# Performance work log

Hardware: AMD Instinct MI355X
Metric: run time of the kernel (lower is better)

## Reference

```python
import jax, jax.numpy as jnp
import numpy as np
from jax import lax
from jax.scipy.special import logsumexp

B, T, H, L = 64, 512, 768, 9


def setup_inputs() -> dict:
    key = jax.random.key(0)
    k1, k2, k3, k4, k5 = jax.random.split(key, 5)
    hidden = jax.random.normal(k1, (B, T, H), dtype=jnp.float32)
    W = jax.random.normal(k2, (L, H), dtype=jnp.float32) * 0.02
    b = jnp.zeros((L,), dtype=jnp.float32)
    transitions = jax.random.normal(k3, (L, L), dtype=jnp.float32) * 0.1
    lengths = jax.random.randint(k4, (B,), T // 2, T + 1)
    seq_mask = jnp.arange(T)[None, :] < lengths[:, None]          # [B,T] bool
    labels = jax.random.randint(k5, (B, T), 0, L).astype(jnp.int32)
    labels = jnp.where(seq_mask, labels, -100).astype(jnp.int32)   # -100 = ignore
    attention_mask = seq_mask.astype(jnp.int32)
    return {"hidden": hidden, "W": W, "b": b, "transitions": transitions,
            "labels": labels, "attention_mask": attention_mask}


def _crf_nll(logits, tags, transitions, mask):
    # numerator: joint score of the gold path (no start/end transitions)
    maskf = mask.astype(logits.dtype)
    emit = jnp.take_along_axis(logits, tags[..., None], axis=2)[..., 0]   # [B,T]
    emit_score = (emit * maskf).sum(-1)
    trans = transitions[tags[:, :-1], tags[:, 1:]]                        # [B,T-1]
    trans_score = (trans * maskf[:, 1:]).sum(-1)
    numerator = emit_score + trans_score
    # denominator: forward algorithm (log-sum-exp recurrence over time)
    def step(alpha, xs):
        logit_t, mask_t = xs                                   # [B,L], [B]
        inner = alpha[:, :, None] + transitions[None, :, :] + logit_t[:, None, :]
        new = logsumexp(inner, axis=1)
        return jnp.where(mask_t[:, None], new, alpha), None
    alpha0 = logits[:, 0]                                      # mask[:,0] assumed True
    alpha, _ = lax.scan(step, alpha0,
                        (jnp.transpose(logits[:, 1:], (1, 0, 2)), mask[:, 1:].T))
    denominator = logsumexp(alpha, axis=-1)
    return -(numerator - denominator).sum()


def _viterbi(logits, transitions, mask):
    num_tags = transitions.shape[0]
    identity_bp = jnp.broadcast_to(jnp.arange(num_tags)[None, :], logits.shape[:1] + (num_tags,))

    def vstep(vscore, xs):
        logit_t, mask_t = xs
        inner = vscore[:, :, None] + transitions[None, :, :]   # [B,L_prev,L_cur]
        bp = jnp.argmax(inner, axis=1)                         # [B,L]
        new = jnp.max(inner, axis=1) + logit_t
        vscore = jnp.where(mask_t[:, None], new, vscore)
        bp = jnp.where(mask_t[:, None], bp, identity_bp)       # carry tag through pad
        return vscore, bp

    vscore0 = logits[:, 0]
    vscore, bps = lax.scan(vstep, vscore0,
                           (jnp.transpose(logits[:, 1:], (1, 0, 2)), mask[:, 1:].T))
    last_tag = jnp.argmax(vscore, axis=-1)                     # [B]

    def btstep(tag, bp_t):
        prev = jnp.take_along_axis(bp_t, tag[:, None], axis=1)[:, 0]
        return prev, tag

    first_tag, tags_rest = lax.scan(btstep, last_tag, bps, reverse=True)  # ys[t]=tag_{t+1}
    return jnp.concatenate([first_tag[:, None], tags_rest.T], axis=1)     # [B,T]


def reference(hidden, W, b, transitions, labels, attention_mask):
    mask = (attention_mask != 0) & (labels != -100)            # create_combined_mask
    logits = jnp.einsum('bth,lh->btl', hidden, W) + b          # classifier (dropout=eval)
    tags = jnp.where(labels == -100, 0, labels)                # adjust_labels_for_crf
    loss = _crf_nll(logits, tags, transitions, mask)           # -log_likelihood (summed)
    vtags = _viterbi(logits, transitions, mask)                # [B,T]
    # pad_predictions: prepend -100, shift right, -100 outside the masked span
    bsz = hidden.shape[0]
    neg = jnp.full((bsz, 1), -100, dtype=jnp.int32)
    shifted = jnp.concatenate([neg, vtags[:, :-1].astype(jnp.int32)], axis=1)
    valid = jnp.concatenate([jnp.zeros((bsz, 1), bool), mask[:, :-1]], axis=1)
    predictions = jnp.where(valid, shifted, -100)
    return loss, predictions
```

## Files before the change

### kernel.cpp

```cpp
#include <hip/hip_runtime.h>

#define BATCH 64
#define TLEN  512
#define HDIM  768
#define LTAGS 9

#define WS_LOGD 0
#define WS_VM   2359296
#define WS_AM   5308416
#define WS_NUMP 5971968


__global__ __launch_bounds__(256) void logits_kernel(
    const float* __restrict__ hidden, const float* __restrict__ W,
    const float* __restrict__ bvec, double* __restrict__ logitsD,
    float* __restrict__ out)
{
    __shared__ float sW[LTAGS * HDIM];
    __shared__ float sb[LTAGS];
    const int tid = threadIdx.x;
    for (int i = tid; i < LTAGS * HDIM; i += 256) sW[i] = W[i];
    if (tid < LTAGS) sb[tid] = bvec[tid];
    if (blockIdx.x == 0 && tid == 0) out[0] = 0.f;
    __syncthreads();

    const int lane = tid & 63;
    const int wave = tid >> 6;
    const int sub  = lane & 7;
    const int rg   = lane >> 3;

    const int B   = blockIdx.x;
    const int res = B & 7, mq = B >> 3;
    const int b   = ((mq >> 3) << 3) + res;
    const int jw  = mq & 7;

    const int rowBase = b * TLEN + jw * 64 + wave * 16;
    const int r0 = rowBase + rg;
    const int r1 = rowBase + rg + 8;
    const float* h0p = hidden + (size_t)r0 * HDIM;
    const float* h1p = hidden + (size_t)r1 * HDIM;

    double acc0[LTAGS], acc1[LTAGS];
    #pragma unroll
    for (int l = 0; l < LTAGS; ++l) { acc0[l] = 0.0; acc1[l] = 0.0; }

    #pragma unroll 2
    for (int i = 0; i < 24; ++i) {
        const int off = i * 32 + sub * 4;
        const float4 h0 = *(const float4*)(h0p + off);
        const float4 h1 = *(const float4*)(h1p + off);
        #pragma unroll
        for (int l = 0; l < LTAGS; ++l) {
            const float4 w = *(const float4*)&sW[l * HDIM + off];
            float d0 = h0.x * w.x;
            d0 = fmaf(h0.y, w.y, d0); d0 = fmaf(h0.z, w.z, d0); d0 = fmaf(h0.w, w.w, d0);
            float d1 = h1.x * w.x;
            d1 = fmaf(h1.y, w.y, d1); d1 = fmaf(h1.z, w.z, d1); d1 = fmaf(h1.w, w.w, d1);
            acc0[l] += (double)d0;
            acc1[l] += (double)d1;
        }
    }
    #pragma unroll
    for (int l = 0; l < LTAGS; ++l) {
        double v0 = acc0[l], v1 = acc1[l];
        #pragma unroll
        for (int off = 4; off > 0; off >>= 1) {
            v0 += __shfl_down(v0, off);
            v1 += __shfl_down(v1, off);
        }
        acc0[l] = v0; acc1[l] = v1;
    }
    if (sub == 0) {
        #pragma unroll
        for (int l = 0; l < LTAGS; ++l) {
            logitsD[(size_t)r0 * LTAGS + l] = acc0[l] + (double)sb[l];
            logitsD[(size_t)r1 * LTAGS + l] = acc1[l] + (double)sb[l];
        }
    }
}

__global__ __launch_bounds__(256) void chunk_kernel(
    const float* __restrict__ trans, const int* __restrict__ labels,
    const int* __restrict__ att, const double* __restrict__ logitsD,
    double* __restrict__ wsVM, float* __restrict__ wsAM,
    double* __restrict__ wsNumP)
{
    __shared__ __align__(16) double sT64[90];
    __shared__ __align__(16) float  sE32[108];
    const int tid = threadIdx.x;
    if (tid < 81) {
        const int k = tid / 9, j = tid - 9 * k;
        float tv = trans[tid];
        sT64[k * 10 + j] = (double)tv;
        sE32[k * 12 + j] = __expf(tv);
    }
    __syncthreads();

    const int B   = blockIdx.x;
    const int res = B & 7, mq = B >> 3;
    const int b   = ((mq >> 3) << 3) + res;
    const int jw  = mq & 7;

    const int* lab = labels + b * TLEN;
    const int* am  = att + b * TLEN;

    if (tid < 72) {
        const int cl = tid / 9, i = tid - 9 * cl;
        const int c  = jw * 8 + cl;

        double M[LTAGS];
        #pragma unroll
        for (int j = 0; j < LTAGS; ++j) M[j] = (i == j) ? 0.0 : -1e300;

        const double* lrow = logitsD + ((size_t)b * TLEN + (c * 8 + 1)) * LTAGS;
        const int t0 = c * 8 + 1;

        double lg[LTAGS], lgN[LTAGS];
        #pragma unroll
        for (int j = 0; j < LTAGS; ++j) lg[j] = lrow[j];
        bool mk = (am[t0] != 0) && (lab[t0] != -100);

        for (int s = 0; s < 8; ++s) {
            bool mkN = false;
            const int tn = t0 + s + 1;
            if (s < 7 && tn <= TLEN - 1) {
                const double* ln = lrow + (s + 1) * LTAGS;
                #pragma unroll
                for (int j = 0; j < LTAGS; ++j) lgN[j] = ln[j];
                mkN = (am[tn] != 0) && (lab[tn] != -100);
            }
            double nw[LTAGS];
            #pragma unroll
            for (int k = 0; k < LTAGS; ++k) {
                const double2* r = (const double2*)&sT64[k * 10];
                const double2 r01 = r[0], r23 = r[1], r45 = r[2], r67 = r[3];
                const double r8 = sT64[k * 10 + 8];
                const double mk64 = M[k];
                if (k == 0) {
                    nw[0] = mk64 + r01.x; nw[1] = mk64 + r01.y;
                    nw[2] = mk64 + r23.x; nw[3] = mk64 + r23.y;
                    nw[4] = mk64 + r45.x; nw[5] = mk64 + r45.y;
                    nw[6] = mk64 + r67.x; nw[7] = mk64 + r67.y;
                    nw[8] = mk64 + r8;
                } else {
                    nw[0] = fmax(nw[0], mk64 + r01.x); nw[1] = fmax(nw[1], mk64 + r01.y);
                    nw[2] = fmax(nw[2], mk64 + r23.x); nw[3] = fmax(nw[3], mk64 + r23.y);
                    nw[4] = fmax(nw[4], mk64 + r45.x); nw[5] = fmax(nw[5], mk64 + r45.y);
                    nw[6] = fmax(nw[6], mk64 + r67.x); nw[7] = fmax(nw[7], mk64 + r67.y);
                    nw[8] = fmax(nw[8], mk64 + r8);
                }
            }
            #pragma unroll
            for (int j = 0; j < LTAGS; ++j) {
                M[j] = mk ? (nw[j] + lg[j]) : M[j];
                lg[j] = lgN[j];
            }
            mk = mkN;
        }
        double* dst = wsVM + ((size_t)b * 64 + c) * 90 + (size_t)i * 10;
        #pragma unroll
        for (int j = 0; j < LTAGS; ++j) dst[j] = M[j];
    } else if (tid >= 128 && tid < 164) {
        const int idx = tid - 128;
        const int cl = idx / 9, i = idx - 9 * cl;
        const int c  = jw * 4 + cl;

        float M[LTAGS];
        #pragma unroll
        for (int j = 0; j < LTAGS; ++j) M[j] = (i == j) ? 0.f : -1e30f;

        const double* lrow = logitsD + ((size_t)b * TLEN + (c * 16 + 1)) * LTAGS;
        const int t0 = c * 16 + 1;

        float lg[LTAGS], lgN[LTAGS];
        #pragma unroll
        for (int j = 0; j < LTAGS; ++j) lg[j] = (float)lrow[j];
        bool mk = (am[t0] != 0) && (lab[t0] != -100);

        for (int s = 0; s < 16; ++s) {
            bool mkN = false;
            const int tn = t0 + s + 1;
            if (s < 15 && tn <= TLEN - 1) {
                const double* ln = lrow + (s + 1) * LTAGS;
                #pragma unroll
                for (int j = 0; j < LTAGS; ++j) lgN[j] = (float)ln[j];
                mkN = (am[tn] != 0) && (lab[tn] != -100);
            }
            float m = M[0];
            #pragma unroll
            for (int k = 1; k < LTAGS; ++k) m = fmaxf(m, M[k]);
            float P[LTAGS];
            #pragma unroll
            for (int k = 0; k < LTAGS; ++k) P[k] = __expf(M[k] - m);
            float sa[LTAGS];
            #pragma unroll
            for (int k = 0; k < LTAGS; ++k) {
                const float4* r = (const float4*)&sE32[k * 12];
                const float4 f03 = r[0], f47 = r[1];
                const float f8 = sE32[k * 12 + 8];
                const float pk = P[k];
                if (k == 0) {
                    sa[0] = pk * f03.x; sa[1] = pk * f03.y; sa[2] = pk * f03.z; sa[3] = pk * f03.w;
                    sa[4] = pk * f47.x; sa[5] = pk * f47.y; sa[6] = pk * f47.z; sa[7] = pk * f47.w;
                    sa[8] = pk * f8;
                } else {
                    sa[0] = fmaf(pk, f03.x, sa[0]); sa[1] = fmaf(pk, f03.y, sa[1]);
                    sa[2] = fmaf(pk, f03.z, sa[2]); sa[3] = fmaf(pk, f03.w, sa[3]);
                    sa[4] = fmaf(pk, f47.x, sa[4]); sa[5] = fmaf(pk, f47.y, sa[5]);
                    sa[6] = fmaf(pk, f47.z, sa[6]); sa[7] = fmaf(pk, f47.w, sa[7]);
                    sa[8] = fmaf(pk, f8,    sa[8]);
                }
            }
            #pragma unroll
            for (int j = 0; j < LTAGS; ++j) {
                float nwj = m + __logf(sa[j]) + lg[j];
                M[j] = mk ? nwj : M[j];
                lg[j] = lgN[j];
            }
            mk = mkN;
        }
        float* dst = wsAM + (((size_t)b * 32 + c) * LTAGS + i) * LTAGS;
        #pragma unroll
        for (int j = 0; j < LTAGS; ++j) dst[j] = M[j];
    } else if (tid >= 192) {
        const int lane = tid - 192;
        const int t = jw * 64 + lane;
        const double* lrowb = logitsD + (size_t)b * TLEN * LTAGS;
        double part = 0.0;
        {
            int lv = lab[t], av = am[t];
            bool mkc = (av != 0) && (lv != -100);
            int tg = (lv == -100) ? 0 : lv;
            if (mkc) part += lrowb[(size_t)t * LTAGS + tg];
            if (t < TLEN - 1) {
                int lv2 = lab[t + 1], av2 = am[t + 1];
                bool mk2 = (av2 != 0) && (lv2 != -100);
                int tg2 = (lv2 == -100) ? 0 : lv2;
                if (mk2) part += sT64[tg * 10 + tg2];
            }
        }
        #pragma unroll
        for (int off = 32; off > 0; off >>= 1) part += __shfl_down(part, off);
        if (lane == 0) wsNumP[b * 8 + jw] = part;
    }
}

__global__ __launch_bounds__(128) void crf2_kernel(
    const float* __restrict__ trans, const int* __restrict__ labels,
    const int* __restrict__ att, const double* __restrict__ logitsD,
    const double* __restrict__ wsVM, const float* __restrict__ wsAM,
    const double* __restrict__ wsNumP, float* __restrict__ out)
{
    __shared__ __align__(16) double sVM[64 * 90];
    __shared__ __align__(16) float  sAM[32 * 81];
    __shared__ __align__(16) double sU[720];
    __shared__ __align__(16) double sT64[90];
    __shared__ unsigned char sMk[513];
    __shared__ int sTagB[65];
    __shared__ double sDen;

    const int b = blockIdx.x, tid = threadIdx.x;
    const int wave = tid >> 6, lane = tid & 63;
    const unsigned long long IDMAP = 0x876543210ull;

    const double2* gVM = (const double2*)(wsVM + (size_t)b * 5760);
    double2* sVM2 = (double2*)sVM;
    for (int i = tid; i < 2880; i += 128) sVM2[i] = gVM[i];
    const float4* gAM = (const float4*)(wsAM + (size_t)b * 2592);
    float4* sAM4 = (float4*)sAM;
    for (int i = tid; i < 648; i += 128) sAM4[i] = gAM[i];

    const int* lab = labels + b * TLEN;
    const int* am  = att + b * TLEN;
    for (int t = tid; t < TLEN; t += 128) {
        int lv = lab[t], av = am[t];
        sMk[t] = (av != 0 && lv != -100) ? 1 : 0;
    }
    if (tid == 0) sMk[TLEN] = 0;
    if (tid < 81) {
        const int k = tid / 9, j = tid - 9 * k;
        sT64[k * 10 + j] = (double)trans[tid];
    }
    __syncthreads();

    double* sSM = sU;
    if (tid < 72) {
        const int g = tid / 9, i = tid - 9 * g;
        double P[LTAGS];
        {
            const double* row = &sVM[(g * 8) * 90 + i * 10];
            #pragma unroll
            for (int j = 0; j < LTAGS; ++j) P[j] = row[j];
        }
        for (int m = g * 8 + 1; m < g * 8 + 8; ++m) {
            double np[LTAGS];
            #pragma unroll
            for (int k = 0; k < LTAGS; ++k) {
                const double2* r = (const double2*)&sVM[m * 90 + k * 10];
                const double2 r01 = r[0], r23 = r[1], r45 = r[2], r67 = r[3];
                const double r8 = sVM[m * 90 + k * 10 + 8];
                const double pk = P[k];
                if (k == 0) {
                    np[0] = pk + r01.x; np[1] = pk + r01.y;
                    np[2] = pk + r23.x; np[3] = pk + r23.y;
                    np[4] = pk + r45.x; np[5] = pk + r45.y;
                    np[6] = pk + r67.x; np[7] = pk + r67.y;
                    np[8] = pk + r8;
                } else {
                    np[0] = fmax(np[0], pk + r01.x); np[1] = fmax(np[1], pk + r01.y);
                    np[2] = fmax(np[2], pk + r23.x); np[3] = fmax(np[3], pk + r23.y);
                    np[4] = fmax(np[4], pk + r45.x); np[5] = fmax(np[5], pk + r45.y);
                    np[6] = fmax(np[6], pk + r67.x); np[7] = fmax(np[7], pk + r67.y);
                    np[8] = fmax(np[8], pk + r8);
                }
            }
            #pragma unroll
            for (int j = 0; j < LTAGS; ++j) P[j] = np[j];
        }
        double* dst = &sSM[g * 90 + i * 10];
        #pragma unroll
        for (int j = 0; j < LTAGS; ++j) dst[j] = P[j];
    }
    __syncthreads();

    unsigned long long* sBPp = (unsigned long long*)sU;
    unsigned long long S = IDMAP;
    int lastTag = 0;

    if (wave == 0) {
        const int c = lane;
        const int myg = c >> 3;
        double v[LTAGS], vS[LTAGS];
        #pragma unroll
        for (int j = 0; j < LTAGS; ++j) v[j] = logitsD[(size_t)b * TLEN * LTAGS + j];

        #pragma unroll
        for (int g = 0; g < 8; ++g) {
            if (g == myg) {
                #pragma unroll
                for (int j = 0; j < LTAGS; ++j) vS[j] = v[j];
            }
            double nv[LTAGS];
            #pragma unroll
            for (int k = 0; k < LTAGS; ++k) {
                const double2* r = (const double2*)&sSM[g * 90 + k * 10];
                const double2 r01 = r[0], r23 = r[1], r45 = r[2], r67 = r[3];
                const double r8 = sSM[g * 90 + k * 10 + 8];
                const double vk = v[k];
                if (k == 0) {
                    nv[0] = vk + r01.x; nv[1] = vk + r01.y;
                    nv[2] = vk + r23.x; nv[3] = vk + r23.y;
                    nv[4] = vk + r45.x; nv[5] = vk + r45.y;
                    nv[6] = vk + r67.x; nv[7] = vk + r67.y;
                    nv[8] = vk + r8;
                } else {
                    nv[0] = fmax(nv[0], vk + r01.x); nv[1] = fmax(nv[1], vk + r01.y);
                    nv[2] = fmax(nv[2], vk + r23.x); nv[3] = fmax(nv[3], vk + r23.y);
                    nv[4] = fmax(nv[4], vk + r45.x); nv[5] = fmax(nv[5], vk + r45.y);
                    nv[6] = fmax(nv[6], vk + r67.x); nv[7] = fmax(nv[7], vk + r67.y);
                    nv[8] = fmax(nv[8], vk + r8);
                }
            }
            #pragma unroll
            for (int j = 0; j < LTAGS; ++j) v[j] = nv[j];
        }
        {
            int bi = 0; double bv = v[0];
            #pragma unroll
            for (int i = 1; i < LTAGS; ++i) if (v[i] > bv) { bv = v[i]; bi = i; }
            lastTag = bi;
        }

        const int nCat = c & 7;
        for (int it = 0; it < nCat; ++it) {
            const int m = (c & ~7) + it;
            double nv[LTAGS];
            #pragma unroll
            for (int k = 0; k < LTAGS; ++k) {
                const double2* r = (const double2*)&sVM[m * 90 + k * 10];
                const double2 r01 = r[0], r23 = r[1], r45 = r[2], r67 = r[3];
                const double r8 = sVM[m * 90 + k * 10 + 8];
                const double vk = vS[k];
                if (k == 0) {
                    nv[0] = vk + r01.x; nv[1] = vk + r01.y;
                    nv[2] = vk + r23.x; nv[3] = vk + r23.y;
                    nv[4] = vk + r45.x; nv[5] = vk + r45.y;
                    nv[6] = vk + r67.x; nv[7] = vk + r67.y;
                    nv[8] = vk + r8;
                } else {
                    nv[0] = fmax(nv[0], vk + r01.x); nv[1] = fmax(nv[1], vk + r01.y);
                    nv[2] = fmax(nv[2], vk + r23.x); nv[3] = fmax(nv[3], vk + r23.y);
                    nv[4] = fmax(nv[4], vk + r45.x); nv[5] = fmax(nv[5], vk + r45.y);
                    nv[6] = fmax(nv[6], vk + r67.x); nv[7] = fmax(nv[7], vk + r67.y);
                    nv[8] = fmax(nv[8], vk + r8);
                }
            }
            #pragma unroll
            for (int j = 0; j < LTAGS; ++j) vS[j] = nv[j];
        }

        const double* lrow = logitsD + ((size_t)b * TLEN + (c * 8 + 1)) * LTAGS;
        double lg[LTAGS], lgN[LTAGS];
        #pragma unroll
        for (int j = 0; j < LTAGS; ++j) lg[j] = lrow[j];

        for (int s = 0; s < 8; ++s) {
            const int t = c * 8 + 1 + s;
            if (s < 7 && t + 1 <= TLEN - 1) {
                const double* ln = lrow + (s + 1) * LTAGS;
                #pragma unroll
                for (int j = 0; j < LTAGS; ++j) lgN[j] = ln[j];
            }
            const bool mk = (sMk[t] != 0);
            double bst[LTAGS];
            int bi[LTAGS];
            #pragma unroll
            for (int k = 0; k < LTAGS; ++k) {
                const double2* r = (const double2*)&sT64[k * 10];
                const double2 r01 = r[0], r23 = r[1], r45 = r[2], r67 = r[3];
                const double r8 = sT64[k * 10 + 8];
                const double vk = vS[k];
                double cnd[LTAGS];
                cnd[0] = vk + r01.x; cnd[1] = vk + r01.y;
                cnd[2] = vk + r23.x; cnd[3] = vk + r23.y;
                cnd[4] = vk + r45.x; cnd[5] = vk + r45.y;
                cnd[6] = vk + r67.x; cnd[7] = vk + r67.y;
                cnd[8] = vk + r8;
                if (k == 0) {
                    #pragma unroll
                    for (int j = 0; j < LTAGS; ++j) { bst[j] = cnd[j]; bi[j] = 0; }
                } else {
                    #pragma unroll
                    for (int j = 0; j < LTAGS; ++j) {
                        bool gt = cnd[j] > bst[j];
                        bst[j] = gt ? cnd[j] : bst[j];
                        bi[j]  = gt ? k : bi[j];
                    }
                }
            }
            unsigned long long pk = 0;
            #pragma unroll
            for (int j = 0; j < LTAGS; ++j)
                pk |= ((unsigned long long)bi[j]) << (4 * j);
            pk = mk ? pk : IDMAP;
            sBPp[t] = pk;
            #pragma unroll
            for (int j = 0; j < LTAGS; ++j) {
                vS[j] = mk ? (bst[j] + lg[j]) : vS[j];
                lg[j] = lgN[j];
            }
        }
        unsigned long long G = IDMAP;
        for (int s = 7; s >= 0; --s) {
            const unsigned long long bp = sBPp[c * 8 + 1 + s];
            unsigned long long ng = 0;
            #pragma unroll
            for (int j = 0; j < LTAGS; ++j) {
                int gj = (int)((G >> (4 * j)) & 15);
                int f  = (int)((bp >> (4 * gj)) & 15);
                ng |= ((unsigned long long)f) << (4 * j);
            }
            G = ng;
        }
        S = G;
    } else {
        const int j = (lane < LTAGS) ? lane : (LTAGS - 1);
        float v = (float)logitsD[(size_t)b * TLEN * LTAGS + j];
        float Mc[LTAGS], Mn[LTAGS];
        #pragma unroll
        for (int i = 0; i < LTAGS; ++i) Mc[i] = sAM[i * LTAGS + j];
        for (int c = 0; c < 32; ++c) {
            if (c < 31) {
                #pragma unroll
                for (int i = 0; i < LTAGS; ++i) Mn[i] = sAM[(c + 1) * 81 + i * LTAGS + j];
            }
            float g[LTAGS];
            #pragma unroll
            for (int i = 0; i < LTAGS; ++i) g[i] = __shfl(v, i);
            float a[LTAGS];
            #pragma unroll
            for (int i = 0; i < LTAGS; ++i) a[i] = g[i] + Mc[i];
            float t01 = fmaxf(a[0], a[1]), t23 = fmaxf(a[2], a[3]);
            float t45 = fmaxf(a[4], a[5]), t67 = fmaxf(a[6], a[7]);
            float m = fmaxf(fmaxf(fmaxf(t01, t23), fmaxf(t45, t67)), a[8]);
            float sacc = 0.f;
            #pragma unroll
            for (int i = 0; i < LTAGS; ++i) sacc += __expf(a[i] - m);
            v = m + __logf(sacc);
            if (c < 31) {
                #pragma unroll
                for (int i = 0; i < LTAGS; ++i) Mc[i] = Mn[i];
            }
        }
        float g[LTAGS];
        #pragma unroll
        for (int i = 0; i < LTAGS; ++i) g[i] = __shfl(v, i);
        if (lane == 0) {
            float m = g[0];
            #pragma unroll
            for (int i = 1; i < LTAGS; ++i) m = fmaxf(m, g[i]);
            float sacc = 0.f;
            #pragma unroll
            for (int i = 0; i < LTAGS; ++i) sacc += __expf(g[i] - m);
            sDen = (double)(m + __logf(sacc));
        }
    }

    #pragma unroll
    for (int d = 1; d < 64; d <<= 1) {
        unsigned long long Sn = __shfl_down(S, d);
        if (wave == 0 && lane + d < 64) {
            unsigned long long R = 0;
            #pragma unroll
            for (int x = 0; x < LTAGS; ++x) {
                int y = (int)((Sn >> (4 * x)) & 15);
                int z = (int)((S >> (4 * y)) & 15);
                R |= ((unsigned long long)z) << (4 * x);
            }
            S = R;
        }
    }
    if (wave == 0) {
        sTagB[tid] = (int)((S >> (4 * lastTag)) & 15);
        if (tid == 0) sTagB[64] = lastTag;
    }
    __syncthreads();

    if (tid < 64) {
        const int c = tid;
        int cur = sTagB[c + 1];
        float* po = out + 1 + b * TLEN;
        for (int s = 8; s >= 1; --s) {
            const int t = c * 8 + s;
            if (t < TLEN) {
                int nxt = (int)((sBPp[t] >> (4 * cur)) & 15);
                po[t] = sMk[t - 1] ? (float)nxt : -100.f;
                cur = nxt;
            }
        }
    }
    if (tid == 0) {
        out[1 + b * TLEN] = -100.f;
        double num = 0.0;
        const double* np = wsNumP + b * 8;
        #pragma unroll
        for (int q = 0; q < 8; ++q) num += np[q];
        atomicAdd(out, (float)(sDen - num));
    }
}

extern "C" void kernel_launch(void* const* d_in, const int* in_sizes, int n_in,
                              void* d_out, int out_size, void* d_ws, size_t ws_size,
                              hipStream_t stream)
{
    const float* hidden = (const float*)d_in[0];
    const float* W      = (const float*)d_in[1];
    const float* bvec   = (const float*)d_in[2];
    const float* trans  = (const float*)d_in[3];
    const int*   labels = (const int*)d_in[4];
    const int*   att    = (const int*)d_in[5];
    float* out = (float*)d_out;

    char* ws = (char*)d_ws;
    double* logitsD = (double*)(ws + WS_LOGD);
    double* wsVM    = (double*)(ws + WS_VM);
    float*  wsAM    = (float*)(ws + WS_AM);
    double* wsNumP  = (double*)(ws + WS_NUMP);

    logits_kernel<<<512, 256, 0, stream>>>(hidden, W, bvec, logitsD, out);
    chunk_kernel<<<512, 256, 0, stream>>>(trans, labels, att, logitsD,
                                          wsVM, wsAM, wsNumP);
    crf2_kernel<<<BATCH, 128, 0, stream>>>(trans, labels, att, logitsD,
                                           wsVM, wsAM, wsNumP, out);
}
```

Before: 219.2 us.

## Fuse chunk and CRF kernels using per-batch flags and in-block prefix products

Merges the chunk kernel and the final CRF kernel into one launch of 576 blocks. The first 512 blocks compute chunk matrices, then build per-group max-plus prefix products and group summaries in shared memory and write them out. They signal completion by atomically incrementing a per-batch flag. The last 64 blocks spin on that flag and then run the sequential Viterbi, forward and backtrace stages using the precomputed prefixes, which removes one launch and the in-block group-composition step. This depends on the producer blocks being scheduled before or alongside the spinning consumers, which risks deadlock or stalls, and it adds global-memory reads of the prefix matrices.

```diff
diff --git a/kernel.cpp b/kernel.cpp
--- a/kernel.cpp
+++ b/kernel.cpp
@@ -6,22 +6,27 @@
 #define LTAGS 9
 
 #define WS_LOGD 0
-#define WS_VM   2359296
-#define WS_AM   5308416
-#define WS_NUMP 5971968
+#define WS_PM   2359296
+#define WS_SM   5308416
+#define WS_AM   5677056
+#define WS_NUMP 6340608
+#define WS_FLAG 6344704
 
 
 __global__ __launch_bounds__(256) void logits_kernel(
     const float* __restrict__ hidden, const float* __restrict__ W,
     const float* __restrict__ bvec, double* __restrict__ logitsD,
-    float* __restrict__ out)
+    unsigned int* __restrict__ flags, float* __restrict__ out)
 {
     __shared__ float sW[LTAGS * HDIM];
     __shared__ float sb[LTAGS];
     const int tid = threadIdx.x;
     for (int i = tid; i < LTAGS * HDIM; i += 256) sW[i] = W[i];
     if (tid < LTAGS) sb[tid] = bvec[tid];
-    if (blockIdx.x == 0 && tid == 0) out[0] = 0.f;
+    if (blockIdx.x == 0) {
+        if (tid < BATCH) flags[tid] = 0u;
+        if (tid == 0) out[0] = 0.f;
+    }
     __syncthreads();
 
     const int lane = tid & 63;
@@ -79,251 +84,254 @@
     }
 }
 
-__global__ __launch_bounds__(256) void chunk_kernel(
+__global__ __launch_bounds__(256) void fused_kernel(
     const float* __restrict__ trans, const int* __restrict__ labels,
     const int* __restrict__ att, const double* __restrict__ logitsD,
-    double* __restrict__ wsVM, float* __restrict__ wsAM,
-    double* __restrict__ wsNumP)
+    double* __restrict__ wsPM, double* __restrict__ wsSM,
+    float* __restrict__ wsAM, double* __restrict__ wsNumP,
+    unsigned int* __restrict__ flags, float* __restrict__ out)
 {
     __shared__ __align__(16) double sT64[90];
     __shared__ __align__(16) float  sE32[108];
-    const int tid = threadIdx.x;
+    __shared__ __align__(16) double sMrow[8 * 90];
+    __shared__ __align__(16) double sSMc[8 * 90];
+    __shared__ __align__(16) float  sAM[32 * 81];
+    __shared__ unsigned long long sBPp[513];
+    __shared__ unsigned char sMk[513];
+    __shared__ int sTagB[65];
+    __shared__ double sDen;
+
+    const int B = blockIdx.x, tid = threadIdx.x;
+    const unsigned long long IDMAP = 0x876543210ull;
+
     if (tid < 81) {
         const int k = tid / 9, j = tid - 9 * k;
         float tv = trans[tid];
         sT64[k * 10 + j] = (double)tv;
         sE32[k * 12 + j] = __expf(tv);
     }
-    __syncthreads();
-
-    const int B   = blockIdx.x;
-    const int res = B & 7, mq = B >> 3;
-    const int b   = ((mq >> 3) << 3) + res;
-    const int jw  = mq & 7;
-
+
+    if (B < 512) {
+        __syncthreads();
+        const int res = B & 7, mq = B >> 3;
+        const int b   = ((mq >> 3) << 3) + res;
+        const int jw  = mq & 7;
+        const int* lab = labels + b * TLEN;
+        const int* am  = att + b * TLEN;
+
+        if (tid < 72) {
+            const int cl = tid / 9, i = tid - 9 * cl;
+            const int c  = jw * 8 + cl;
+
+            double M[LTAGS];
+            #pragma unroll
+            for (int j = 0; j < LTAGS; ++j) M[j] = (i == j) ? 0.0 : -1e300;
+
+            const double* lrow = logitsD + ((size_t)b * TLEN + (c * 8 + 1)) * LTAGS;
+            const int t0 = c * 8 + 1;
+
+            double lg[LTAGS], lgN[LTAGS];
+            #pragma unroll
+            for (int j = 0; j < LTAGS; ++j) lg[j] = lrow[j];
+            bool mk = (am[t0] != 0) && (lab[t0] != -100);
+
+            for (int s = 0; s < 8; ++s) {
+                bool mkN = false;
+                const int tn = t0 + s + 1;
+                if (s < 7 && tn <= TLEN - 1) {
+                    const double* ln = lrow + (s + 1) * LTAGS;
+                    #pragma unroll
+                    for (int j = 0; j < LTAGS; ++j) lgN[j] = ln[j];
+                    mkN = (am[tn] != 0) && (lab[tn] != -100);
+                }
+                double nw[LTAGS];
+                #pragma unroll
+                for (int k = 0; k < LTAGS; ++k) {
+                    const double2* r = (const double2*)&sT64[k * 10];
+                    const double2 r01 = r[0], r23 = r[1], r45 = r[2], r67 = r[3];
+                    const double r8 = sT64[k * 10 + 8];
+                    const double mk64 = M[k];
+                    if (k == 0) {
+                        nw[0] = mk64 + r01.x; nw[1] = mk64 + r01.y;
+                        nw[2] = mk64 + r23.x; nw[3] = mk64 + r23.y;
+                        nw[4] = mk64 + r45.x; nw[5] = mk64 + r45.y;
+                        nw[6] = mk64 + r67.x; nw[7] = mk64 + r67.y;
+                        nw[8] = mk64 + r8;
+                    } else {
+                        nw[0] = fmax(nw[0], mk64 + r01.x); nw[1] = fmax(nw[1], mk64 + r01.y);
+                        nw[2] = fmax(nw[2], mk64 + r23.x); nw[3] = fmax(nw[3], mk64 + r23.y);
+                        nw[4] = fmax(nw[4], mk64 + r45.x); nw[5] = fmax(nw[5], mk64 + r45.y);
+                        nw[6] = fmax(nw[6], mk64 + r67.x); nw[7] = fmax(nw[7], mk64 + r67.y);
+                        nw[8] = fmax(nw[8], mk64 + r8);
+                    }
+                }
+                #pragma unroll
+                for (int j = 0; j < LTAGS; ++j) {
+                    M[j] = mk ? (nw[j] + lg[j]) : M[j];
+                    lg[j] = lgN[j];
+                }
+                mk = mkN;
+            }
+            double* dst = &sMrow[cl * 90 + i * 10];
+            #pragma unroll
+            for (int j = 0; j < LTAGS; ++j) dst[j] = M[j];
+        } else if (tid >= 128 && tid < 164) {
+            const int idx = tid - 128;
+            const int cl = idx / 9, i = idx - 9 * cl;
+            const int c  = jw * 4 + cl;
+
+            float M[LTAGS];
+            #pragma unroll
+            for (int j = 0; j < LTAGS; ++j) M[j] = (i == j) ? 0.f : -1e30f;
+
+            const double* lrow = logitsD + ((size_t)b * TLEN + (c * 16 + 1)) * LTAGS;
+            const int t0 = c * 16 + 1;
+
+            float lg[LTAGS], lgN[LTAGS];
+            #pragma unroll
+            for (int j = 0; j < LTAGS; ++j) lg[j] = (float)lrow[j];
+            bool mk = (am[t0] != 0) && (lab[t0] != -100);
+
+            for (int s = 0; s < 16; ++s) {
+                bool mkN = false;
+                const int tn = t0 + s + 1;
+                if (s < 15 && tn <= TLEN - 1) {
+                    const double* ln = lrow + (s + 1) * LTAGS;
+                    #pragma unroll
+                    for (int j = 0; j < LTAGS; ++j) lgN[j] = (float)ln[j];
+                    mkN = (am[tn] != 0) && (lab[tn] != -100);
+                }
+                float m = M[0];
+                #pragma unroll
+                for (int k = 1; k < LTAGS; ++k) m = fmaxf(m, M[k]);
+                float P[LTAGS];
+                #pragma unroll
+                for (int k = 0; k < LTAGS; ++k) P[k] = __expf(M[k] - m);
+                float sa[LTAGS];
+                #pragma unroll
+                for (int k = 0; k < LTAGS; ++k) {
+                    const float4* r = (const float4*)&sE32[k * 12];
+                    const float4 f03 = r[0], f47 = r[1];
+                    const float f8 = sE32[k * 12 + 8];
+                    const float pk = P[k];
+                    if (k == 0) {
+                        sa[0] = pk * f03.x; sa[1] = pk * f03.y; sa[2] = pk * f03.z; sa[3] = pk * f03.w;
+                        sa[4] = pk * f47.x; sa[5] = pk * f47.y; sa[6] = pk * f47.z; sa[7] = pk * f47.w;
+                        sa[8] = pk * f8;
+                    } else {
+                        sa[0] = fmaf(pk, f03.x, sa[0]); sa[1] = fmaf(pk, f03.y, sa[1]);
+                        sa[2] = fmaf(pk, f03.z, sa[2]); sa[3] = fmaf(pk, f03.w, sa[3]);
+                        sa[4] = fmaf(pk, f47.x, sa[4]); sa[5] = fmaf(pk, f47.y, sa[5]);
+                        sa[6] = fmaf(pk, f47.z, sa[6]); sa[7] = fmaf(pk, f47.w, sa[7]);
+                        sa[8] = fmaf(pk, f8,    sa[8]);
+                    }
+                }
+                #pragma unroll
+                for (int j = 0; j < LTAGS; ++j) {
+                    float nwj = m + __logf(sa[j]) + lg[j];
+                    M[j] = mk ? nwj : M[j];
+                    lg[j] = lgN[j];
+                }
+                mk = mkN;
+            }
+            float* dst = wsAM + (((size_t)b * 32 + c) * LTAGS + i) * LTAGS;
+            #pragma unroll
+            for (int j = 0; j < LTAGS; ++j) dst[j] = M[j];
+        } else if (tid >= 192) {
+            const int lane = tid - 192;
+            const int t = jw * 64 + lane;
+            const double* lrowb = logitsD + (size_t)b * TLEN * LTAGS;
+            double part = 0.0;
+            {
+                int lv = lab[t], av = am[t];
+                bool mkc = (av != 0) && (lv != -100);
+                int tg = (lv == -100) ? 0 : lv;
+                if (mkc) part += lrowb[(size_t)t * LTAGS + tg];
+                if (t < TLEN - 1) {
+                    int lv2 = lab[t + 1], av2 = am[t + 1];
+                    bool mk2 = (av2 != 0) && (lv2 != -100);
+                    int tg2 = (lv2 == -100) ? 0 : lv2;
+                    if (mk2) part += sT64[tg * 10 + tg2];
+                }
+            }
+            #pragma unroll
+            for (int off = 32; off > 0; off >>= 1) part += __shfl_down(part, off);
+            if (lane == 0) wsNumP[b * 8 + jw] = part;
+        }
+        __syncthreads();
+
+        if (tid < 9) {
+            const int i = tid;
+            double P[LTAGS];
+            #pragma unroll
+            for (int j = 0; j < LTAGS; ++j) P[j] = (i == j) ? 0.0 : -1e300;
+            double* basePM = wsPM + (((size_t)b * 8 + jw) * 8) * 90;
+            for (int l = 0; l < 8; ++l) {
+                double* dst = basePM + (size_t)l * 90 + i * 10;
+                #pragma unroll
+                for (int j = 0; j < LTAGS; ++j) dst[j] = P[j];
+                double np[LTAGS];
+                #pragma unroll
+                for (int k = 0; k < LTAGS; ++k) {
+                    const double2* r = (const double2*)&sMrow[l * 90 + k * 10];
+                    const double2 r01 = r[0], r23 = r[1], r45 = r[2], r67 = r[3];
+                    const double r8 = sMrow[l * 90 + k * 10 + 8];
+                    const double pk = P[k];
+                    if (k == 0) {
+                        np[0] = pk + r01.x; np[1] = pk + r01.y;
+                        np[2] = pk + r23.x; np[3] = pk + r23.y;
+                        np[4] = pk + r45.x; np[5] = pk + r45.y;
+                        np[6] = pk + r67.x; np[7] = pk + r67.y;
+                        np[8] = pk + r8;
+                    } else {
+                        np[0] = fmax(np[0], pk + r01.x); np[1] = fmax(np[1], pk + r01.y);
+                        np[2] = fmax(np[2], pk + r23.x); np[3] = fmax(np[3], pk + r23.y);
+                        np[4] = fmax(np[4], pk + r45.x); np[5] = fmax(np[5], pk + r45.y);
+                        np[6] = fmax(np[6], pk + r67.x); np[7] = fmax(np[7], pk + r67.y);
+                        np[8] = fmax(np[8], pk + r8);
+                    }
+                }
+                #pragma unroll
+                for (int j = 0; j < LTAGS; ++j) P[j] = np[j];
+            }
+            double* dstS = wsSM + ((size_t)b * 8 + jw) * 90 + i * 10;
+            #pragma unroll
+            for (int j = 0; j < LTAGS; ++j) dstS[j] = P[j];
+        }
+        __syncthreads();
+        if (tid == 0)
+            __hip_atomic_fetch_add(&flags[b], 1u, __ATOMIC_RELEASE,
+                                   __HIP_MEMORY_SCOPE_AGENT);
+        return;
+    }
+
+    const int b = B - 512;
+    const int wave = tid >> 6, lane = tid & 63;
     const int* lab = labels + b * TLEN;
     const int* am  = att + b * TLEN;
 
-    if (tid < 72) {
-        const int cl = tid / 9, i = tid - 9 * cl;
-        const int c  = jw * 8 + cl;
-
-        double M[LTAGS];
-        #pragma unroll
-        for (int j = 0; j < LTAGS; ++j) M[j] = (i == j) ? 0.0 : -1e300;
-
-        const double* lrow = logitsD + ((size_t)b * TLEN + (c * 8 + 1)) * LTAGS;
-        const int t0 = c * 8 + 1;
-
-        double lg[LTAGS], lgN[LTAGS];
-        #pragma unroll
-        for (int j = 0; j < LTAGS; ++j) lg[j] = lrow[j];
-        bool mk = (am[t0] != 0) && (lab[t0] != -100);
-
-        for (int s = 0; s < 8; ++s) {
-            bool mkN = false;
-            const int tn = t0 + s + 1;
-            if (s < 7 && tn <= TLEN - 1) {
-                const double* ln = lrow + (s + 1) * LTAGS;
-                #pragma unroll
-                for (int j = 0; j < LTAGS; ++j) lgN[j] = ln[j];
-                mkN = (am[tn] != 0) && (lab[tn] != -100);
-            }
-            double nw[LTAGS];
-            #pragma unroll
-            for (int k = 0; k < LTAGS; ++k) {
-                const double2* r = (const double2*)&sT64[k * 10];
-                const double2 r01 = r[0], r23 = r[1], r45 = r[2], r67 = r[3];
-                const double r8 = sT64[k * 10 + 8];
-                const double mk64 = M[k];
-                if (k == 0) {
-                    nw[0] = mk64 + r01.x; nw[1] = mk64 + r01.y;
-                    nw[2] = mk64 + r23.x; nw[3] = mk64 + r23.y;
-                    nw[4] = mk64 + r45.x; nw[5] = mk64 + r45.y;
-                    nw[6] = mk64 + r67.x; nw[7] = mk64 + r67.y;
-                    nw[8] = mk64 + r8;
-                } else {
-                    nw[0] = fmax(nw[0], mk64 + r01.x); nw[1] = fmax(nw[1], mk64 + r01.y);
-                    nw[2] = fmax(nw[2], mk64 + r23.x); nw[3] = fmax(nw[3], mk64 + r23.y);
-                    nw[4] = fmax(nw[4], mk64 + r45.x); nw[5] = fmax(nw[5], mk64 + r45.y);
-                    nw[6] = fmax(nw[6], mk64 + r67.x); nw[7] = fmax(nw[7], mk64 + r67.y);
-                    nw[8] = fmax(nw[8], mk64 + r8);
-                }
-            }
-            #pragma unroll
-            for (int j = 0; j < LTAGS; ++j) {
-                M[j] = mk ? (nw[j] + lg[j]) : M[j];
-                lg[j] = lgN[j];
-            }
-            mk = mkN;
-        }
-        double* dst = wsVM + ((size_t)b * 64 + c) * 90 + (size_t)i * 10;
-        #pragma unroll
-        for (int j = 0; j < LTAGS; ++j) dst[j] = M[j];
-    } else if (tid >= 128 && tid < 164) {
-        const int idx = tid - 128;
-        const int cl = idx / 9, i = idx - 9 * cl;
-        const int c  = jw * 4 + cl;
-
-        float M[LTAGS];
-        #pragma unroll
-        for (int j = 0; j < LTAGS; ++j) M[j] = (i == j) ? 0.f : -1e30f;
-
-        const double* lrow = logitsD + ((size_t)b * TLEN + (c * 16 + 1)) * LTAGS;
-        const int t0 = c * 16 + 1;
-
-        float lg[LTAGS], lgN[LTAGS];
-        #pragma unroll
-        for (int j = 0; j < LTAGS; ++j) lg[j] = (float)lrow[j];
-        bool mk = (am[t0] != 0) && (lab[t0] != -100);
-
-        for (int s = 0; s < 16; ++s) {
-            bool mkN = false;
-            const int tn = t0 + s + 1;
-            if (s < 15 && tn <= TLEN - 1) {
-                const double* ln = lrow + (s + 1) * LTAGS;
-                #pragma unroll
-                for (int j = 0; j < LTAGS; ++j) lgN[j] = (float)ln[j];
-                mkN = (am[tn] != 0) && (lab[tn] != -100);
-            }
-            float m = M[0];
-            #pragma unroll
-            for (int k = 1; k < LTAGS; ++k) m = fmaxf(m, M[k]);
-            float P[LTAGS];
-            #pragma unroll
-            for (int k = 0; k < LTAGS; ++k) P[k] = __expf(M[k] - m);
-            float sa[LTAGS];
-            #pragma unroll
-            for (int k = 0; k < LTAGS; ++k) {
-                const float4* r = (const float4*)&sE32[k * 12];
-                const float4 f03 = r[0], f47 = r[1];
-                const float f8 = sE32[k * 12 + 8];
-                const float pk = P[k];
-                if (k == 0) {
-                    sa[0] = pk * f03.x; sa[1] = pk * f03.y; sa[2] = pk * f03.z; sa[3] = pk * f03.w;
-                    sa[4] = pk * f47.x; sa[5] = pk * f47.y; sa[6] = pk * f47.z; sa[7] = pk * f47.w;
-                    sa[8] = pk * f8;
-                } else {
-                    sa[0] = fmaf(pk, f03.x, sa[0]); sa[1] = fmaf(pk, f03.y, sa[1]);
-                    sa[2] = fmaf(pk, f03.z, sa[2]); sa[3] = fmaf(pk, f03.w, sa[3]);
-                    sa[4] = fmaf(pk, f47.x, sa[4]); sa[5] = fmaf(pk, f47.y, sa[5]);
-                    sa[6] = fmaf(pk, f47.z, sa[6]); sa[7] = fmaf(pk, f47.w, sa[7]);
-                    sa[8] = fmaf(pk, f8,    sa[8]);
-                }
-            }
-            #pragma unroll
-            for (int j = 0; j < LTAGS; ++j) {
-                float nwj = m + __logf(sa[j]) + lg[j];
-                M[j] = mk ? nwj : M[j];
-                lg[j] = lgN[j];
-            }
-            mk = mkN;
-        }
-        float* dst = wsAM + (((size_t)b * 32 + c) * LTAGS + i) * LTAGS;
-        #pragma unroll
-        for (int j = 0; j < LTAGS; ++j) dst[j] = M[j];
-    } else if (tid >= 192) {
-        const int lane = tid - 192;
-        const int t = jw * 64 + lane;
-        const double* lrowb = logitsD + (size_t)b * TLEN * LTAGS;
-        double part = 0.0;
-        {
-            int lv = lab[t], av = am[t];
-            bool mkc = (av != 0) && (lv != -100);
-            int tg = (lv == -100) ? 0 : lv;
-            if (mkc) part += lrowb[(size_t)t * LTAGS + tg];
-            if (t < TLEN - 1) {
-                int lv2 = lab[t + 1], av2 = am[t + 1];
-                bool mk2 = (av2 != 0) && (lv2 != -100);
-                int tg2 = (lv2 == -100) ? 0 : lv2;
-                if (mk2) part += sT64[tg * 10 + tg2];
-            }
-        }
-        #pragma unroll
-        for (int off = 32; off > 0; off >>= 1) part += __shfl_down(part, off);
-        if (lane == 0) wsNumP[b * 8 + jw] = part;
-    }
-}
-
-__global__ __launch_bounds__(128) void crf2_kernel(
-    const float* __restrict__ trans, const int* __restrict__ labels,
-    const int* __restrict__ att, const double* __restrict__ logitsD,
-    const double* __restrict__ wsVM, const float* __restrict__ wsAM,
-    const double* __restrict__ wsNumP, float* __restrict__ out)
-{
-    __shared__ __align__(16) double sVM[64 * 90];
-    __shared__ __align__(16) float  sAM[32 * 81];
-    __shared__ __align__(16) double sU[720];
-    __shared__ __align__(16) double sT64[90];
-    __shared__ unsigned char sMk[513];
-    __shared__ int sTagB[65];
-    __shared__ double sDen;
-
-    const int b = blockIdx.x, tid = threadIdx.x;
-    const int wave = tid >> 6, lane = tid & 63;
-    const unsigned long long IDMAP = 0x876543210ull;
-
-    const double2* gVM = (const double2*)(wsVM + (size_t)b * 5760);
-    double2* sVM2 = (double2*)sVM;
-    for (int i = tid; i < 2880; i += 128) sVM2[i] = gVM[i];
-    const float4* gAM = (const float4*)(wsAM + (size_t)b * 2592);
-    float4* sAM4 = (float4*)sAM;
-    for (int i = tid; i < 648; i += 128) sAM4[i] = gAM[i];
-
-    const int* lab = labels + b * TLEN;
-    const int* am  = att + b * TLEN;
-    for (int t = tid; t < TLEN; t += 128) {
+    for (int t = tid; t < TLEN; t += 256) {
         int lv = lab[t], av = am[t];
         sMk[t] = (av != 0 && lv != -100) ? 1 : 0;
     }
     if (tid == 0) sMk[TLEN] = 0;
-    if (tid < 81) {
-        const int k = tid / 9, j = tid - 9 * k;
-        sT64[k * 10 + j] = (double)trans[tid];
-    }
     __syncthreads();
 
-    double* sSM = sU;
-    if (tid < 72) {
-        const int g = tid / 9, i = tid - 9 * g;
-        double P[LTAGS];
-        {
-            const double* row = &sVM[(g * 8) * 90 + i * 10];
-            #pragma unroll
-            for (int j = 0; j < LTAGS; ++j) P[j] = row[j];
-        }
-        for (int m = g * 8 + 1; m < g * 8 + 8; ++m) {
-            double np[LTAGS];
-            #pragma unroll
-            for (int k = 0; k < LTAGS; ++k) {
-                const double2* r = (const double2*)&sVM[m * 90 + k * 10];
-                const double2 r01 = r[0], r23 = r[1], r45 = r[2], r67 = r[3];
-                const double r8 = sVM[m * 90 + k * 10 + 8];
-                const double pk = P[k];
-                if (k == 0) {
-                    np[0] = pk + r01.x; np[1] = pk + r01.y;
-                    np[2] = pk + r23.x; np[3] = pk + r23.y;
-                    np[4] = pk + r45.x; np[5] = pk + r45.y;
-                    np[6] = pk + r67.x; np[7] = pk + r67.y;
-                    np[8] = pk + r8;
-                } else {
-                    np[0] = fmax(np[0], pk + r01.x); np[1] = fmax(np[1], pk + r01.y);
-                    np[2] = fmax(np[2], pk + r23.x); np[3] = fmax(np[3], pk + r23.y);
-                    np[4] = fmax(np[4], pk + r45.x); np[5] = fmax(np[5], pk + r45.y);
-                    np[6] = fmax(np[6], pk + r67.x); np[7] = fmax(np[7], pk + r67.y);
-                    np[8] = fmax(np[8], pk + r8);
-                }
-            }
-            #pragma unroll
-            for (int j = 0; j < LTAGS; ++j) P[j] = np[j];
-        }
-        double* dst = &sSM[g * 90 + i * 10];
-        #pragma unroll
-        for (int j = 0; j < LTAGS; ++j) dst[j] = P[j];
-    }
+    while (__hip_atomic_load(&flags[b], __ATOMIC_ACQUIRE,
+                             __HIP_MEMORY_SCOPE_AGENT) != 8u)
+        __builtin_amdgcn_s_sleep(2);
     __syncthreads();
 
-    unsigned long long* sBPp = (unsigned long long*)sU;
+    {
+        const double2* gSM = (const double2*)(wsSM + (size_t)b * 720);
+        double2* sSM2 = (double2*)sSMc;
+        for (int i = tid; i < 360; i += 256) sSM2[i] = gSM[i];
+        const float4* gAM = (const float4*)(wsAM + (size_t)b * 2592);
+        float4* sAM4 = (float4*)sAM;
+        for (int i = tid; i < 648; i += 256) sAM4[i] = gAM[i];
+    }
+    __syncthreads();
+
     unsigned long long S = IDMAP;
     int lastTag = 0;
 
@@ -343,9 +351,9 @@
             double nv[LTAGS];
             #pragma unroll
             for (int k = 0; k < LTAGS; ++k) {
-                const double2* r = (const double2*)&sSM[g * 90 + k * 10];
+                const double2* r = (const double2*)&sSMc[g * 90 + k * 10];
                 const double2 r01 = r[0], r23 = r[1], r45 = r[2], r67 = r[3];
-                const double r8 = sSM[g * 90 + k * 10 + 8];
+                const double r8 = sSMc[g * 90 + k * 10 + 8];
                 const double vk = v[k];
                 if (k == 0) {
                     nv[0] = vk + r01.x; nv[1] = vk + r01.y;
@@ -371,15 +379,15 @@
             lastTag = bi;
         }
 
-        const int nCat = c & 7;
-        for (int it = 0; it < nCat; ++it) {
-            const int m = (c & ~7) + it;
+        const int l = c & 7;
+        if (l) {
+            const double* pm = wsPM + (((size_t)b * 8 + myg) * 8 + l) * 90;
             double nv[LTAGS];
             #pragma unroll
             for (int k = 0; k < LTAGS; ++k) {
-                const double2* r = (const double2*)&sVM[m * 90 + k * 10];
+                const double2* r = (const double2*)&pm[k * 10];
                 const double2 r01 = r[0], r23 = r[1], r45 = r[2], r67 = r[3];
-                const double r8 = sVM[m * 90 + k * 10 + 8];
+                const double r8 = pm[k * 10 + 8];
                 const double vk = vS[k];
                 if (k == 0) {
                     nv[0] = vk + r01.x; nv[1] = vk + r01.y;
@@ -463,7 +471,7 @@
             G = ng;
         }
         S = G;
-    } else {
+    } else if (wave == 1) {
         const int j = (lane < LTAGS) ? lane : (LTAGS - 1);
         float v = (float)logitsD[(size_t)b * TLEN * LTAGS + j];
         float Mc[LTAGS], Mn[LTAGS];
@@ -563,13 +571,13 @@
 
     char* ws = (char*)d_ws;
     double* logitsD = (double*)(ws + WS_LOGD);
-    double* wsVM    = (double*)(ws + WS_VM);
+    double* wsPM    = (double*)(ws + WS_PM);
+    double* wsSM    = (double*)(ws + WS_SM);
     float*  wsAM    = (float*)(ws + WS_AM);
     double* wsNumP  = (double*)(ws + WS_NUMP);
-
-    logits_kernel<<<512, 256, 0, stream>>>(hidden, W, bvec, logitsD, out);
-    chunk_kernel<<<512, 256, 0, stream>>>(trans, labels, att, logitsD,
-                                          wsVM, wsAM, wsNumP);
-    crf2_kernel<<<BATCH, 128, 0, stream>>>(trans, labels, att, logitsD,
-                                           wsVM, wsAM, wsNumP, out);
+    unsigned int* flags = (unsigned int*)(ws + WS_FLAG);
+
+    logits_kernel<<<512, 256, 0, stream>>>(hidden, W, bvec, logitsD, flags, out);
+    fused_kernel<<<576, 256, 0, stream>>>(trans, labels, att, logitsD,
+                                          wsPM, wsSM, wsAM, wsNumP, flags, out);
 }
```

After: 239.5 us. 9.3% more time.
